# Performance work log

Measured on AMD Instinct MI355X. Metric: run time of the kernel, lower is better.

Reference implementation:

```python
import jax, jax.numpy as jnp
import numpy as np

N_EMBD = 768
N_HEAD = 12
N_KV_HEAD = 4                      # repeat factor in _repeat_kv
NUM_KV_HEADS = N_HEAD // N_KV_HEAD # 3 actual kv heads
HEAD_DIM = N_EMBD // N_HEAD        # 64
BLOCK_SIZE = 1024                  # sliding window size
SCALE = (HEAD_DIM * N_KV_HEAD / N_HEAD) ** (-0.5)


def _rotary_cos_sin(T, d, dtype):
    inv_freq = 1.0 / (10000.0 ** (jnp.arange(0, d, 2, dtype=jnp.float32) / d))
    t = jnp.arange(T, dtype=jnp.float32)
    freqs = jnp.outer(t, inv_freq)  # (T, d/2)
    return jnp.cos(freqs).astype(dtype)[None, None], jnp.sin(freqs).astype(dtype)[None, None]


def _apply_rotary(x):
    # x: (b, h, T, d)
    T, d = x.shape[2], x.shape[3]
    cos, sin = _rotary_cos_sin(T, d, x.dtype)
    x1, x2 = x[..., : d // 2], x[..., d // 2 :]
    return jnp.concatenate([x1 * cos - x2 * sin, x1 * sin + x2 * cos], axis=-1)


def setup_inputs() -> dict:
    key = jax.random.key(0)
    k0, k1, k2, k3, k4 = jax.random.split(key, 5)
    b, T = 2, 2048
    s = 0.02
    return {
        "hidden_states": jax.random.normal(k0, (b, T, N_EMBD), jnp.float32),
        "Wq": jax.random.normal(k1, (N_HEAD * HEAD_DIM, N_EMBD), jnp.float32) * s,
        "Wk": jax.random.normal(k2, (NUM_KV_HEADS * HEAD_DIM, N_EMBD), jnp.float32) * s,
        "Wv": jax.random.normal(k3, (NUM_KV_HEADS * HEAD_DIM, N_EMBD), jnp.float32) * s,
        "Wo": jax.random.normal(k4, (N_EMBD, N_HEAD * HEAD_DIM), jnp.float32) * s,
    }


def reference(hidden_states, Wq, Wk, Wv, Wo):
    b, T, _ = hidden_states.shape
    q = (hidden_states @ Wq.T).reshape(b, T, N_HEAD, HEAD_DIM).transpose(0, 2, 1, 3)
    k = (hidden_states @ Wk.T).reshape(b, T, NUM_KV_HEADS, HEAD_DIM).transpose(0, 2, 1, 3)
    v = (hidden_states @ Wv.T).reshape(b, T, NUM_KV_HEADS, HEAD_DIM).transpose(0, 2, 1, 3)

    # _repeat_kv: each kv head repeated n_kv_head (=4) times contiguously
    k = jnp.repeat(k, N_KV_HEAD, axis=1)
    v = jnp.repeat(v, N_KV_HEAD, axis=1)

    q = _apply_rotary(q)
    k = _apply_rotary(k)

    # centered sliding-window mask (faithful to per-token loop):
    # window_start = clip(i - W//2, 0, T - W); window is always exactly W wide
    W = BLOCK_SIZE
    i = jnp.arange(T)[:, None]
    j = jnp.arange(T)[None, :]
    start = jnp.clip(i - W // 2, 0, T - W)
    mask = (j >= start) & (j < start + W)  # (T, T)

    scores = jnp.einsum("bhqd,bhkd->bhqk", q, k) * SCALE
    scores = jnp.where(mask[None, None], scores, jnp.finfo(scores.dtype).min)
    attn = jax.nn.softmax(scores, axis=-1)
    out = jnp.einsum("bhqk,bhkd->bhqd", attn, v)  # (b, h, T, d)

    out = out.transpose(0, 2, 1, 3).reshape(b, T, N_EMBD)
    return out @ Wo.T
```

## Files before the change

### kernel.cpp

```cpp
#include <hip/hip_runtime.h>
#include <math.h>

#define T_SEQ 2048
#define E 768
#define WIN 1024
#define KDIM 768
#define HS_SZ ((size_t)4096 * 768)
#define SCALE 0.21650635094610965f

typedef _Float16 f16x8 __attribute__((ext_vector_type(8)));
typedef _Float16 f16x4 __attribute__((ext_vector_type(4)));
typedef float f32x4 __attribute__((ext_vector_type(4)));
typedef __attribute__((address_space(3))) _Float16 lf16;

#define MFMA16(a, b, c) __builtin_amdgcn_mfma_f32_16x16x32_f16(a, b, c, 0, 0, 0)

__device__ __forceinline__ void dma16(const _Float16* g, lf16* l) {
    __builtin_amdgcn_global_load_lds(
        (const __attribute__((address_space(1))) void*)g,
        (__attribute__((address_space(3))) void*)l, 16, 0, 0);
}

__device__ __forceinline__ void cast8(const float* __restrict__ src,
                                      _Float16* __restrict__ dst, int i) {
    float4 a = *(const float4*)&src[i];
    float4 b = *(const float4*)&src[i + 4];
    f16x8 h;
    h[0] = (_Float16)a.x; h[1] = (_Float16)a.y; h[2] = (_Float16)a.z; h[3] = (_Float16)a.w;
    h[4] = (_Float16)b.x; h[5] = (_Float16)b.y; h[6] = (_Float16)b.z; h[7] = (_Float16)b.w;
    *(f16x8*)&dst[i] = h;
}

__global__ __launch_bounds__(256) void prep(
    const float* __restrict__ hs,
    const float* __restrict__ Wq, const float* __restrict__ Wk,
    const float* __restrict__ Wv, const float* __restrict__ Wo,
    _Float16* __restrict__ hs16,
    _Float16* __restrict__ Wq16, _Float16* __restrict__ Wk16,
    _Float16* __restrict__ Wv16, _Float16* __restrict__ Wo16,
    float2* __restrict__ rtab) {
    int tid = blockIdx.x * 256 + threadIdx.x;
    int i = tid * 8;
    if (i < 768 * 768) { cast8(Wq, Wq16, i); cast8(Wo, Wo16, i); }
    if (i < 192 * 768) { cast8(Wk, Wk16, i); cast8(Wv, Wv16, i); }
    cast8(hs, hs16, i);
    if (tid < 2048 * 32) {
        int t = tid >> 5, d = tid & 31;
        float inv = powf(10000.0f, -(float)(2 * d) * (1.0f / 64.0f));
        float s, c;
        sincosf((float)t * inv, &s, &c);
        rtab[tid] = make_float2(c, s);
    }
}

__global__ __launch_bounds__(256) void gemm_qkv(
    const _Float16* __restrict__ A16,
    const _Float16* __restrict__ Wq16, const _Float16* __restrict__ Wk16,
    const _Float16* __restrict__ Wv16, const float2* __restrict__ rtab,
    _Float16* __restrict__ q16, _Float16* __restrict__ k16,
    _Float16* __restrict__ vT16) {
    __shared__ __align__(16) _Float16 As[128 * 64];
    __shared__ __align__(16) _Float16 Bs[64 * 64];
    const int tid = threadIdx.x;
    const int bx = blockIdx.x;
    const int m0 = blockIdx.y * 128;
    const int w = tid >> 6, lane = tid & 63;
    const int mm = lane & 15, quad = lane >> 4;

    const _Float16* bbase; int brb;
    if (bx < 12)      { bbase = Wq16; brb = bx * 64; }
    else if (bx < 15) { bbase = Wk16; brb = (bx - 12) * 64; }
    else              { bbase = Wv16; brb = (bx - 15) * 64; }

    const int rofs = lane >> 3;
    const int gsw = ((lane & 7) ^ rofs) * 8;

    const _Float16* agp[4]; lf16* alp[4];
    #pragma unroll
    for (int j = 0; j < 4; ++j) {
        int c = j * 4 + w;
        agp[j] = A16 + (size_t)(m0 + c * 8 + rofs) * KDIM + gsw;
        alp[j] = ((lf16*)As) + c * 512 + lane * 8;
    }
    const _Float16* bgp[2]; lf16* blp[2];
    #pragma unroll
    for (int j = 0; j < 2; ++j) {
        int c = j * 4 + w;
        bgp[j] = bbase + (size_t)(brb + c * 8 + rofs) * KDIM + gsw;
        blp[j] = ((lf16*)Bs) + c * 512 + lane * 8;
    }

    f32x4 acc[2][4] = {};
    const int xr = mm & 7;

    for (int it = 0; it < 12; ++it) {
        const int ke = it * 64;
        __syncthreads();
        #pragma unroll
        for (int j = 0; j < 4; ++j) dma16(agp[j] + ke, alp[j]);
        #pragma unroll
        for (int j = 0; j < 2; ++j) dma16(bgp[j] + ke, blp[j]);
        __syncthreads();
        #pragma unroll
        for (int s = 0; s < 2; ++s) {
            const int gq = ((s * 4 + quad) ^ xr) * 8;
            f16x8 ah[2];
            #pragma unroll
            for (int mt = 0; mt < 2; ++mt)
                ah[mt] = *(const f16x8*)&As[(w * 32 + mt * 16 + mm) * 64 + gq];
            #pragma unroll
            for (int nt = 0; nt < 4; ++nt) {
                f16x8 bh = *(const f16x8*)&Bs[(nt * 16 + mm) * 64 + gq];
                #pragma unroll
                for (int mt = 0; mt < 2; ++mt)
                    acc[mt][nt] = MFMA16(ah[mt], bh, acc[mt][nt]);
            }
        }
    }

    #pragma unroll
    for (int mt = 0; mt < 2; ++mt) {
        #pragma unroll
        for (int r = 0; r < 4; ++r) {
            int row = m0 + w * 32 + mt * 16 + quad * 4 + r;
            int t = row & (T_SEQ - 1);
            int b = row >> 11;
            if (bx < 12) {
                _Float16* dst = &q16[(size_t)row * E + bx * 64 + mm];
                #pragma unroll
                for (int nt = 0; nt < 2; ++nt) {
                    int d = nt * 16 + mm;
                    float2 cs = rtab[t * 32 + d];
                    float x1 = acc[mt][nt][r], x2 = acc[mt][nt + 2][r];
                    dst[nt * 16]       = (_Float16)((x1 * cs.x - x2 * cs.y) * SCALE);
                    dst[(nt + 2) * 16] = (_Float16)((x1 * cs.y + x2 * cs.x) * SCALE);
                }
            } else if (bx < 15) {
                int kvh = bx - 12;
                _Float16* dst = &k16[(((size_t)(b * 3 + kvh)) * T_SEQ + t) * 64 + mm];
                #pragma unroll
                for (int nt = 0; nt < 2; ++nt) {
                    int d = nt * 16 + mm;
                    float2 cs = rtab[t * 32 + d];
                    float x1 = acc[mt][nt][r], x2 = acc[mt][nt + 2][r];
                    dst[nt * 16]       = (_Float16)(x1 * cs.x - x2 * cs.y);
                    dst[(nt + 2) * 16] = (_Float16)(x1 * cs.y + x2 * cs.x);
                }
            } else {
                int kvh = bx - 15;
                #pragma unroll
                for (int nt = 0; nt < 4; ++nt) {
                    int d = nt * 16 + mm;
                    vT16[(((size_t)(b * 3 + kvh)) * 64 + d) * T_SEQ + t] = (_Float16)acc[mt][nt][r];
                }
            }
        }
    }
}

__global__ __launch_bounds__(256) void gemm_out(
    const _Float16* __restrict__ A16, const _Float16* __restrict__ B16,
    float* __restrict__ C) {
    __shared__ __align__(16) _Float16 As[128 * 64];
    __shared__ __align__(16) _Float16 Bs[64 * 64];
    const int tid = threadIdx.x;
    const int n0 = blockIdx.x * 64;
    const int m0 = blockIdx.y * 128;
    const int w = tid >> 6, lane = tid & 63;
    const int mm = lane & 15, quad = lane >> 4;

    const int rofs = lane >> 3;
    const int gsw = ((lane & 7) ^ rofs) * 8;

    const _Float16* agp[4]; lf16* alp[4];
    #pragma unroll
    for (int j = 0; j < 4; ++j) {
        int c = j * 4 + w;
        agp[j] = A16 + (size_t)(m0 + c * 8 + rofs) * KDIM + gsw;
        alp[j] = ((lf16*)As) + c * 512 + lane * 8;
    }
    const _Float16* bgp[2]; lf16* blp[2];
    #pragma unroll
    for (int j = 0; j < 2; ++j) {
        int c = j * 4 + w;
        bgp[j] = B16 + (size_t)(n0 + c * 8 + rofs) * KDIM + gsw;
        blp[j] = ((lf16*)Bs) + c * 512 + lane * 8;
    }

    f32x4 acc[2][4] = {};
    const int xr = mm & 7;

    for (int it = 0; it < 12; ++it) {
        const int ke = it * 64;
        __syncthreads();
        #pragma unroll
        for (int j = 0; j < 4; ++j) dma16(agp[j] + ke, alp[j]);
        #pragma unroll
        for (int j = 0; j < 2; ++j) dma16(bgp[j] + ke, blp[j]);
        __syncthreads();
        #pragma unroll
        for (int s = 0; s < 2; ++s) {
            const int gq = ((s * 4 + quad) ^ xr) * 8;
            f16x8 ah[2];
            #pragma unroll
            for (int mt = 0; mt < 2; ++mt)
                ah[mt] = *(const f16x8*)&As[(w * 32 + mt * 16 + mm) * 64 + gq];
            #pragma unroll
            for (int nt = 0; nt < 4; ++nt) {
                f16x8 bh = *(const f16x8*)&Bs[(nt * 16 + mm) * 64 + gq];
                #pragma unroll
                for (int mt = 0; mt < 2; ++mt)
                    acc[mt][nt] = MFMA16(ah[mt], bh, acc[mt][nt]);
            }
        }
    }
    #pragma unroll
    for (int mt = 0; mt < 2; ++mt)
        #pragma unroll
        for (int r = 0; r < 4; ++r) {
            int row = m0 + w * 32 + mt * 16 + quad * 4 + r;
            float* cp = &C[(size_t)row * 768 + n0 + mm];
            #pragma unroll
            for (int nt = 0; nt < 4; ++nt)
                cp[nt * 16] = acc[mt][nt][r];
        }
}

__global__ __launch_bounds__(256) void attn_mfma(const _Float16* __restrict__ q16,
                                                 const _Float16* __restrict__ k16,
                                                 const _Float16* __restrict__ vT16,
                                                 _Float16* __restrict__ aout16) {
    __shared__ __align__(16) char smem[8192 + 8192 + 10240];
    _Float16* k_s  = (_Float16*)smem;
    _Float16* vT_s = (_Float16*)(smem + 8192);
    _Float16 (*p_s)[40] = (_Float16(*)[40])(smem + 16384);
    float* ored = (float*)smem;
    float* lred = (float*)(smem + 16384);

    const int b = blockIdx.z, h = blockIdx.y;
    const int i0 = blockIdx.x * 64;
    const int plane = b * 3 + (h >> 2);
    const int tid = threadIdx.x;
    const int w = tid >> 6, lane = tid & 63;
    const int m = lane & 15, quad = lane >> 4;
    const int qh = w & 1, kh = w >> 1;
    const int xm = m & 7;

    int s0 = i0 - 512;      s0 = s0 < 0 ? 0 : (s0 > 1024 ? 1024 : s0);
    int sL = i0 + 63 - 512; sL = sL < 0 ? 0 : (sL > 1024 ? 1024 : sL);
    const int nc = (sL + WIN - s0 + 63) >> 6;

    int start_q[2];
    f16x8 qf[2][2];
    #pragma unroll
    for (int qt = 0; qt < 2; ++qt) {
        int qi = i0 + qh * 32 + qt * 16 + m;
        int sq = qi - 512; sq = sq < 0 ? 0 : (sq > 1024 ? 1024 : sq);
        start_q[qt] = sq;
        const _Float16* qp = &q16[((size_t)(b * T_SEQ + qi)) * E + h * 64 + quad * 8];
        qf[qt][0] = *(const f16x8*)&qp[0];
        qf[qt][1] = *(const f16x8*)&qp[32];
    }

    f32x4 o[2][4] = {};
    float l_run[2] = {0.0f, 0.0f};

    const int rofs = lane >> 3;
    const int glog = (lane & 7) ^ rofs;
    const _Float16* kg[2]; lf16* kl[2];
    const _Float16* vg[2]; lf16* vl[2];
    #pragma unroll
    for (int j = 0; j < 2; ++j) {
        int rr = (j * 4 + w) * 8 + rofs;
        kg[j] = k16 + ((size_t)plane * T_SEQ + rr) * 64 + glog * 8;
        kl[j] = ((lf16*)k_s) + ((j * 4 + w) * 64 + lane) * 8;
        vg[j] = vT16 + ((size_t)plane * 64 + rr) * T_SEQ + glog * 8;
        vl[j] = ((lf16*)vT_s) + ((j * 4 + w) * 64 + lane) * 8;
    }

    for (int ci = 0; ci < nc; ++ci) {
        const int c0 = s0 + ci * 64;
        __syncthreads();
        dma16(kg[0] + (size_t)c0 * 64, kl[0]);
        dma16(kg[1] + (size_t)c0 * 64, kl[1]);
        dma16(vg[0] + c0, vl[0]);
        dma16(vg[1] + c0, vl[1]);
        __syncthreads();

        f32x4 st[2][2] = {};
        #pragma unroll
        for (int s = 0; s < 2; ++s) {
            #pragma unroll
            for (int kt = 0; kt < 2; ++kt) {
                int row = kh * 32 + kt * 16 + m;
                int g = (s * 4 + quad) ^ xm;
                f16x8 a = *(const f16x8*)&k_s[row * 64 + g * 8];
                #pragma unroll
                for (int qt = 0; qt < 2; ++qt)
                    st[kt][qt] = MFMA16(a, qf[qt][s], st[kt][qt]);
            }
        }

        const bool boundary = (c0 < sL) || (c0 + 63 > s0 + 1023);
        if (boundary) {
            #pragma unroll
            for (int kt = 0; kt < 2; ++kt)
                #pragma unroll
                for (int qt = 0; qt < 2; ++qt)
                    #pragma unroll
                    for (int r = 0; r < 4; ++r) {
                        int j = c0 + kh * 32 + kt * 16 + quad * 4 + r;
                        bool valid = (j >= start_q[qt]) && (j < start_q[qt] + WIN);
                        st[kt][qt][r] = valid ? st[kt][qt][r] : -INFINITY;
                    }
        }

        #pragma unroll
        for (int kt = 0; kt < 2; ++kt)
            #pragma unroll
            for (int qt = 0; qt < 2; ++qt) {
                float p0 = __expf(st[kt][qt][0]);
                float p1 = __expf(st[kt][qt][1]);
                float p2 = __expf(st[kt][qt][2]);
                float p3 = __expf(st[kt][qt][3]);
                l_run[qt] += (p0 + p1) + (p2 + p3);
                f16x4 pv = {(_Float16)p0, (_Float16)p1, (_Float16)p2, (_Float16)p3};
                *(f16x4*)&p_s[w * 32 + qt * 16 + m][kt * 16 + quad * 4] = pv;
            }

        f16x8 bp[2];
        #pragma unroll
        for (int qt = 0; qt < 2; ++qt)
            bp[qt] = *(const f16x8*)&p_s[w * 32 + qt * 16 + m][quad * 8];
        #pragma unroll
        for (int mt = 0; mt < 4; ++mt) {
            int g = (kh * 4 + quad) ^ xm;
            f16x8 a = *(const f16x8*)&vT_s[(mt * 16 + m) * 64 + g * 8];
            #pragma unroll
            for (int qt = 0; qt < 2; ++qt)
                o[qt][mt] = MFMA16(a, bp[qt], o[qt][mt]);
        }
    }

    float l_tot[2];
    #pragma unroll
    for (int qt = 0; qt < 2; ++qt) {
        float l = l_run[qt];
        l += __shfl_xor(l, 16);
        l += __shfl_xor(l, 32);
        l_tot[qt] = l;
    }

    __syncthreads();
    if (kh == 1) {
        #pragma unroll
        for (int qt = 0; qt < 2; ++qt) {
            #pragma unroll
            for (int mt = 0; mt < 4; ++mt) {
                int idx = ((qh * 32 + qt * 16 + m) << 6) + mt * 16 + quad * 4;
                *(float4*)&ored[idx] = *(float4*)&o[qt][mt];
            }
            if (quad == 0) lred[qh * 32 + qt * 16 + m] = l_tot[qt];
        }
    }
    __syncthreads();
    if (kh == 0) {
        #pragma unroll
        for (int qt = 0; qt < 2; ++qt) {
            float rl = 1.0f / (l_tot[qt] + lred[qh * 32 + qt * 16 + m]);
            int qi = i0 + qh * 32 + qt * 16 + m;
            _Float16* op = &aout16[((size_t)(b * T_SEQ + qi)) * E + h * 64];
            #pragma unroll
            for (int mt = 0; mt < 4; ++mt) {
                int idx = ((qh * 32 + qt * 16 + m) << 6) + mt * 16 + quad * 4;
                float4 other = *(float4*)&ored[idx];
                #pragma unroll
                for (int r = 0; r < 4; ++r) {
                    float x = (o[qt][mt][r] + (&other.x)[r]) * rl;
                    op[mt * 16 + quad * 4 + r] = (_Float16)x;
                }
            }
        }
    }
}

extern "C" void kernel_launch(void* const* d_in, const int* in_sizes, int n_in,
                              void* d_out, int out_size, void* d_ws, size_t ws_size,
                              hipStream_t stream) {
    const float* hs = (const float*)d_in[0];
    const float* Wq = (const float*)d_in[1];
    const float* Wk = (const float*)d_in[2];
    const float* Wv = (const float*)d_in[3];
    const float* Wo = (const float*)d_in[4];
    float* out = (float*)d_out;

    _Float16* hs16   = (_Float16*)d_ws;
    _Float16* aout16 = hs16 + HS_SZ;
    _Float16* q16    = aout16 + HS_SZ;
    _Float16* k16    = q16 + HS_SZ;
    _Float16* vT16   = k16 + 6 * 2048 * 64;
    _Float16* Wq16   = vT16 + 6 * 2048 * 64;
    _Float16* Wk16   = Wq16 + 768 * 768;
    _Float16* Wv16   = Wk16 + 192 * 768;
    _Float16* Wo16   = Wv16 + 192 * 768;
    float2*   rtab   = (float2*)(Wo16 + 768 * 768);

    dim3 blk(256);
    prep<<<dim3((int)(HS_SZ / 8 / 256)), blk, 0, stream>>>(hs, Wq, Wk, Wv, Wo,
                                                           hs16, Wq16, Wk16, Wv16, Wo16, rtab);
    gemm_qkv<<<dim3(18, 32), blk, 0, stream>>>(hs16, Wq16, Wk16, Wv16, rtab, q16, k16, vT16);
    attn_mfma<<<dim3(32, 12, 2), blk, 0, stream>>>(q16, k16, vT16, aout16);
    gemm_out<<<dim3(12, 32), blk, 0, stream>>>(aout16, Wo16, out);
}
```

Measured before the change: 136.2 us.

## Widen GEMM K-tiles, shrink out-proj tile, register-prefetch K/V in attention

Both GEMMs now stage 128-wide K slices with a 16-way XOR swizzle, halving the number of barrier-separated load steps. The output projection uses 64x64 tiles with a 2x2 warp layout, doubling the grid to fill more CUs. The attention kernel replaces direct global-to-LDS DMA with register prefetch of the next K/V chunk, so global loads overlap compute. The cost is more LDS per block and more registers, which may lower occupancy.

```diff
diff --git a/kernel.cpp b/kernel.cpp
--- a/kernel.cpp
+++ b/kernel.cpp
@@ -59,8 +59,8 @@
     const _Float16* __restrict__ Wv16, const float2* __restrict__ rtab,
     _Float16* __restrict__ q16, _Float16* __restrict__ k16,
     _Float16* __restrict__ vT16) {
-    __shared__ __align__(16) _Float16 As[128 * 64];
-    __shared__ __align__(16) _Float16 Bs[64 * 64];
+    __shared__ __align__(16) _Float16 As[128 * 128];
+    __shared__ __align__(16) _Float16 Bs[64 * 128];
     const int tid = threadIdx.x;
     const int bx = blockIdx.x;
     const int m0 = blockIdx.y * 128;
@@ -72,45 +72,48 @@
     else if (bx < 15) { bbase = Wk16; brb = (bx - 12) * 64; }
     else              { bbase = Wv16; brb = (bx - 15) * 64; }
 
-    const int rofs = lane >> 3;
-    const int gsw = ((lane & 7) ^ rofs) * 8;
-
-    const _Float16* agp[4]; lf16* alp[4];
+    const int rofs4 = lane >> 4;
+    const int gs = lane & 15;
+
+    const _Float16* agp[8]; lf16* alp[8];
+    #pragma unroll
+    for (int j = 0; j < 8; ++j) {
+        int c = j * 4 + w;
+        int rr = c * 4 + rofs4;
+        int glog = gs ^ (rr & 15);
+        agp[j] = A16 + (size_t)(m0 + rr) * KDIM + glog * 8;
+        alp[j] = ((lf16*)As) + c * 512 + lane * 8;
+    }
+    const _Float16* bgp[4]; lf16* blp[4];
     #pragma unroll
     for (int j = 0; j < 4; ++j) {
         int c = j * 4 + w;
-        agp[j] = A16 + (size_t)(m0 + c * 8 + rofs) * KDIM + gsw;
-        alp[j] = ((lf16*)As) + c * 512 + lane * 8;
-    }
-    const _Float16* bgp[2]; lf16* blp[2];
-    #pragma unroll
-    for (int j = 0; j < 2; ++j) {
-        int c = j * 4 + w;
-        bgp[j] = bbase + (size_t)(brb + c * 8 + rofs) * KDIM + gsw;
+        int rr = c * 4 + rofs4;
+        int glog = gs ^ (rr & 15);
+        bgp[j] = bbase + (size_t)(brb + rr) * KDIM + glog * 8;
         blp[j] = ((lf16*)Bs) + c * 512 + lane * 8;
     }
 
     f32x4 acc[2][4] = {};
-    const int xr = mm & 7;
-
-    for (int it = 0; it < 12; ++it) {
-        const int ke = it * 64;
-        __syncthreads();
-        #pragma unroll
-        for (int j = 0; j < 4; ++j) dma16(agp[j] + ke, alp[j]);
-        #pragma unroll
-        for (int j = 0; j < 2; ++j) dma16(bgp[j] + ke, blp[j]);
-        __syncthreads();
-        #pragma unroll
-        for (int s = 0; s < 2; ++s) {
-            const int gq = ((s * 4 + quad) ^ xr) * 8;
+
+    for (int it = 0; it < 6; ++it) {
+        const int ke = it * 128;
+        __syncthreads();
+        #pragma unroll
+        for (int j = 0; j < 8; ++j) dma16(agp[j] + ke, alp[j]);
+        #pragma unroll
+        for (int j = 0; j < 4; ++j) dma16(bgp[j] + ke, blp[j]);
+        __syncthreads();
+        #pragma unroll
+        for (int s = 0; s < 4; ++s) {
+            const int gq = ((s * 4 + quad) ^ mm) * 8;
             f16x8 ah[2];
             #pragma unroll
             for (int mt = 0; mt < 2; ++mt)
-                ah[mt] = *(const f16x8*)&As[(w * 32 + mt * 16 + mm) * 64 + gq];
+                ah[mt] = *(const f16x8*)&As[(w * 32 + mt * 16 + mm) * 128 + gq];
             #pragma unroll
             for (int nt = 0; nt < 4; ++nt) {
-                f16x8 bh = *(const f16x8*)&Bs[(nt * 16 + mm) * 64 + gq];
+                f16x8 bh = *(const f16x8*)&Bs[(nt * 16 + mm) * 128 + gq];
                 #pragma unroll
                 for (int mt = 0; mt < 2; ++mt)
                     acc[mt][nt] = MFMA16(ah[mt], bh, acc[mt][nt]);
@@ -161,67 +164,66 @@
 __global__ __launch_bounds__(256) void gemm_out(
     const _Float16* __restrict__ A16, const _Float16* __restrict__ B16,
     float* __restrict__ C) {
-    __shared__ __align__(16) _Float16 As[128 * 64];
-    __shared__ __align__(16) _Float16 Bs[64 * 64];
+    __shared__ __align__(16) _Float16 As[64 * 128];
+    __shared__ __align__(16) _Float16 Bs[64 * 128];
     const int tid = threadIdx.x;
     const int n0 = blockIdx.x * 64;
-    const int m0 = blockIdx.y * 128;
+    const int m0 = blockIdx.y * 64;
     const int w = tid >> 6, lane = tid & 63;
     const int mm = lane & 15, quad = lane >> 4;
-
-    const int rofs = lane >> 3;
-    const int gsw = ((lane & 7) ^ rofs) * 8;
+    const int wm = (w & 1) * 32, wn = (w >> 1) * 32;
+
+    const int rofs4 = lane >> 4;
+    const int gs = lane & 15;
 
     const _Float16* agp[4]; lf16* alp[4];
+    const _Float16* bgp[4]; lf16* blp[4];
     #pragma unroll
     for (int j = 0; j < 4; ++j) {
         int c = j * 4 + w;
-        agp[j] = A16 + (size_t)(m0 + c * 8 + rofs) * KDIM + gsw;
+        int rr = c * 4 + rofs4;
+        int glog = gs ^ (rr & 15);
+        agp[j] = A16 + (size_t)(m0 + rr) * KDIM + glog * 8;
         alp[j] = ((lf16*)As) + c * 512 + lane * 8;
-    }
-    const _Float16* bgp[2]; lf16* blp[2];
-    #pragma unroll
-    for (int j = 0; j < 2; ++j) {
-        int c = j * 4 + w;
-        bgp[j] = B16 + (size_t)(n0 + c * 8 + rofs) * KDIM + gsw;
+        bgp[j] = B16 + (size_t)(n0 + rr) * KDIM + glog * 8;
         blp[j] = ((lf16*)Bs) + c * 512 + lane * 8;
     }
 
-    f32x4 acc[2][4] = {};
-    const int xr = mm & 7;
-
-    for (int it = 0; it < 12; ++it) {
-        const int ke = it * 64;
+    f32x4 acc[2][2] = {};
+
+    for (int it = 0; it < 6; ++it) {
+        const int ke = it * 128;
         __syncthreads();
         #pragma unroll
         for (int j = 0; j < 4; ++j) dma16(agp[j] + ke, alp[j]);
         #pragma unroll
-        for (int j = 0; j < 2; ++j) dma16(bgp[j] + ke, blp[j]);
-        __syncthreads();
-        #pragma unroll
-        for (int s = 0; s < 2; ++s) {
-            const int gq = ((s * 4 + quad) ^ xr) * 8;
-            f16x8 ah[2];
+        for (int j = 0; j < 4; ++j) dma16(bgp[j] + ke, blp[j]);
+        __syncthreads();
+        #pragma unroll
+        for (int s = 0; s < 4; ++s) {
+            const int gq = ((s * 4 + quad) ^ mm) * 8;
+            f16x8 ah[2], bh[2];
             #pragma unroll
             for (int mt = 0; mt < 2; ++mt)
-                ah[mt] = *(const f16x8*)&As[(w * 32 + mt * 16 + mm) * 64 + gq];
-            #pragma unroll
-            for (int nt = 0; nt < 4; ++nt) {
-                f16x8 bh = *(const f16x8*)&Bs[(nt * 16 + mm) * 64 + gq];
+                ah[mt] = *(const f16x8*)&As[(wm + mt * 16 + mm) * 128 + gq];
+            #pragma unroll
+            for (int nt = 0; nt < 2; ++nt)
+                bh[nt] = *(const f16x8*)&Bs[(wn + nt * 16 + mm) * 128 + gq];
+            #pragma unroll
+            for (int nt = 0; nt < 2; ++nt)
                 #pragma unroll
                 for (int mt = 0; mt < 2; ++mt)
-                    acc[mt][nt] = MFMA16(ah[mt], bh, acc[mt][nt]);
-            }
+                    acc[mt][nt] = MFMA16(ah[mt], bh[nt], acc[mt][nt]);
         }
     }
     #pragma unroll
     for (int mt = 0; mt < 2; ++mt)
         #pragma unroll
         for (int r = 0; r < 4; ++r) {
-            int row = m0 + w * 32 + mt * 16 + quad * 4 + r;
-            float* cp = &C[(size_t)row * 768 + n0 + mm];
-            #pragma unroll
-            for (int nt = 0; nt < 4; ++nt)
+            int row = m0 + wm + mt * 16 + quad * 4 + r;
+            float* cp = &C[(size_t)row * 768 + n0 + wn + mm];
+            #pragma unroll
+            for (int nt = 0; nt < 2; ++nt)
                 cp[nt * 16] = acc[mt][nt][r];
         }
 }
@@ -267,25 +269,41 @@
 
     const int rofs = lane >> 3;
     const int glog = (lane & 7) ^ rofs;
-    const _Float16* kg[2]; lf16* kl[2];
-    const _Float16* vg[2]; lf16* vl[2];
+    const _Float16* kgb[2]; const _Float16* vgb[2];
+    _Float16* klw[2]; _Float16* vlw[2];
     #pragma unroll
     for (int j = 0; j < 2; ++j) {
         int rr = (j * 4 + w) * 8 + rofs;
-        kg[j] = k16 + ((size_t)plane * T_SEQ + rr) * 64 + glog * 8;
-        kl[j] = ((lf16*)k_s) + ((j * 4 + w) * 64 + lane) * 8;
-        vg[j] = vT16 + ((size_t)plane * 64 + rr) * T_SEQ + glog * 8;
-        vl[j] = ((lf16*)vT_s) + ((j * 4 + w) * 64 + lane) * 8;
+        kgb[j] = k16 + ((size_t)plane * T_SEQ + rr) * 64 + glog * 8;
+        vgb[j] = vT16 + ((size_t)plane * 64 + rr) * T_SEQ + glog * 8;
+        klw[j] = k_s + (j * 4 + w) * 512 + lane * 8;
+        vlw[j] = vT_s + (j * 4 + w) * 512 + lane * 8;
+    }
+
+    f16x8 kr[2], vr[2];
+    #pragma unroll
+    for (int j = 0; j < 2; ++j) {
+        kr[j] = *(const f16x8*)(kgb[j] + (size_t)s0 * 64);
+        vr[j] = *(const f16x8*)(vgb[j] + s0);
     }
 
     for (int ci = 0; ci < nc; ++ci) {
         const int c0 = s0 + ci * 64;
         __syncthreads();
-        dma16(kg[0] + (size_t)c0 * 64, kl[0]);
-        dma16(kg[1] + (size_t)c0 * 64, kl[1]);
-        dma16(vg[0] + c0, vl[0]);
-        dma16(vg[1] + c0, vl[1]);
-        __syncthreads();
+        #pragma unroll
+        for (int j = 0; j < 2; ++j) {
+            *(f16x8*)klw[j] = kr[j];
+            *(f16x8*)vlw[j] = vr[j];
+        }
+        __syncthreads();
+        if (ci + 1 < nc) {
+            const int cn = c0 + 64;
+            #pragma unroll
+            for (int j = 0; j < 2; ++j) {
+                kr[j] = *(const f16x8*)(kgb[j] + (size_t)cn * 64);
+                vr[j] = *(const f16x8*)(vgb[j] + cn);
+            }
+        }
 
         f32x4 st[2][2] = {};
         #pragma unroll
@@ -410,5 +428,5 @@
                                                            hs16, Wq16, Wk16, Wv16, Wo16, rtab);
     gemm_qkv<<<dim3(18, 32), blk, 0, stream>>>(hs16, Wq16, Wk16, Wv16, rtab, q16, k16, vT16);
     attn_mfma<<<dim3(32, 12, 2), blk, 0, stream>>>(q16, k16, vT16, aout16);
-    gemm_out<<<dim3(12, 32), blk, 0, stream>>>(aout16, Wo16, out);
-}
+    gemm_out<<<dim3(12, 64), blk, 0, stream>>>(aout16, Wo16, out);
+}
```

Measured after the change: 135.3 us (median of 2 runs). About the same (-0.7%).
